# Optimization experiments

Measured on AMD Instinct MI355X. Metric: run time of the kernel, lower is better.

Reference implementation:

```python
import jax, jax.numpy as jnp
import numpy as np

N_NODES = 50000
N_EDGES = 800000
D = 64
LN_EPS = 1e-5


def setup_inputs() -> dict:
    key = jax.random.key(0)
    k1, k2, k3 = jax.random.split(key, 3)
    x = jax.random.normal(k1, (N_NODES, D), dtype=jnp.float32)
    edge_index = jax.random.randint(k2, (2, N_EDGES), 0, N_NODES, dtype=jnp.int64)
    # GCNConv linear weight (no bias in lin; conv bias separate), kaiming-ish scale
    W = jax.random.normal(k3, (D, D), dtype=jnp.float32) / np.sqrt(D)
    b = jnp.zeros((D,), dtype=jnp.float32)
    # LayerNorm affine params
    gamma = jnp.ones((D,), dtype=jnp.float32)
    beta = jnp.zeros((D,), dtype=jnp.float32)
    return {"x": x, "edge_index": edge_index, "W": W, "b": b, "gamma": gamma, "beta": beta}


def reference(x, edge_index, W, b, gamma, beta):
    n = x.shape[0]
    # --- GCNConv (normalize=True, improved=False, add_self_loops=True) ---
    loops = jnp.arange(n, dtype=edge_index.dtype)
    src = jnp.concatenate([edge_index[0], loops])  # message sources j
    dst = jnp.concatenate([edge_index[1], loops])  # message targets i
    ew = jnp.ones(src.shape[0], dtype=x.dtype)
    deg = jax.ops.segment_sum(ew, dst, num_segments=n)          # in-degree incl. self-loop
    dinv = jnp.where(deg > 0, jax.lax.rsqrt(jnp.where(deg > 0, deg, 1.0)), 0.0)
    norm = dinv[src] * dinv[dst]                                 # [E+N]
    xw = x @ W                                                   # [N, D]
    z = jax.ops.segment_sum(norm[:, None] * xw[src], dst, num_segments=n) + b
    # --- identity skip connection ---
    h = x + z
    # --- norm_act_drop: LayerNorm + ReLU (dropout_prob=0) ---
    mu = jnp.mean(h, axis=-1, keepdims=True)
    var = jnp.mean((h - mu) ** 2, axis=-1, keepdims=True)
    hn = (h - mu) * jax.lax.rsqrt(var + LN_EPS)
    return jax.nn.relu(hn * gamma + beta)
```

## Files before the change

### kernel.cpp

```cpp
#include <hip/hip_runtime.h>
#include <hip/hip_fp16.h>

#define N_NODES 50000
#define N_EDGES 800000
#define D 64
#define LN_EPS 1e-5f
#define CAP 48
#define SENT 50000
#define PREP_NB ((N_EDGES / 4 + 255) / 256)
#define GEMM_NB ((N_NODES + 63) / 64)
#define CNT_PAD 50048
#define XS_ROWS 50008
#define NRG 8
#define RSPAN2 6250
#define NCH2 64
#define CHSZ2 12500
#define SC_EB 782

typedef unsigned short u16;
typedef unsigned int u32;


__global__ __launch_bounds__(256) void prep_gemm_k(const int* __restrict__ src,
                                                   const int* __restrict__ dst,
                                                   u32* __restrict__ pe,
                                                   const float* __restrict__ x,
                                                   const float* __restrict__ W,
                                                   __half* __restrict__ xs) {
    __shared__ float xlds[D * D];
    int bid = blockIdx.x;
    int tid = threadIdx.x;
    if (bid < PREP_NB) {
        int gid = bid * 256 + tid;
        if (gid < N_EDGES / 4) {
            int4 s = ((const int4*)src)[gid];
            int4 d = ((const int4*)dst)[gid];
            uint4 p;
            p.x = (u32)(u16)d.x | ((u32)(u16)s.x << 16);
            p.y = (u32)(u16)d.y | ((u32)(u16)s.y << 16);
            p.z = (u32)(u16)d.z | ((u32)(u16)s.z << 16);
            p.w = (u32)(u16)d.w | ((u32)(u16)s.w << 16);
            ((uint4*)pe)[gid] = p;
        }
    } else {
        int row0 = (bid - PREP_NB) * 64;
        const float4* xg = (const float4*)(x + (size_t)row0 * D);
        float4* xl4 = (float4*)xlds;
        for (int i = tid; i < D * D / 4; i += 256) {
            int grow = row0 + (i >> 4);
            xl4[i] = (grow < N_NODES) ? xg[i] : make_float4(0.f, 0.f, 0.f, 0.f);
        }
        int lane = tid & 63;
        float wcol[D];
#pragma unroll
        for (int k = 0; k < D; ++k) wcol[k] = W[k * D + lane];
        __syncthreads();
        int wv = tid >> 6;
        for (int rr = 0; rr < 16; ++rr) {
            int r = wv * 16 + rr;
            int grow = row0 + r;
            if (grow >= N_NODES + 1) break;
            const float4* xr = (const float4*)(xlds + r * D);
            float acc = 0.f;
#pragma unroll
            for (int k4 = 0; k4 < 16; ++k4) {
                float4 xv = xr[k4];
                acc += xv.x * wcol[k4 * 4 + 0];
                acc += xv.y * wcol[k4 * 4 + 1];
                acc += xv.z * wcol[k4 * 4 + 2];
                acc += xv.w * wcol[k4 * 4 + 3];
            }
            xs[(size_t)grow * D + lane] = __float2half(acc);
        }
    }
}

__global__ __launch_bounds__(256) void hist_k(const u32* __restrict__ pe,
                                              u16* __restrict__ lpos,
                                              u16* __restrict__ H) {
    __shared__ u32 lh[RSPAN2];
    int r = blockIdx.x & (NRG - 1);
    int c = blockIdx.x >> 3;
    int lo = r * RSPAN2;
    for (int w = threadIdx.x; w < RSPAN2; w += 256) lh[w] = 0;
    __syncthreads();
    int cbase = c * CHSZ2;
    for (int i = 0; i < 49; ++i) {
        int e = cbase + i * 256 + threadIdx.x;
        if (e < cbase + CHSZ2) {
            u32 p = pe[e];
            unsigned tr = (p & 0xffffu) - (unsigned)lo;
            if (tr < RSPAN2) {
                u32 old = atomicAdd(&lh[tr], 1u);
                lpos[e] = (u16)old;
            }
        }
    }
    __syncthreads();
    u32* H32 = (u32*)(H + (size_t)c * N_NODES + lo);
    for (int w = threadIdx.x; w < RSPAN2 / 2; w += 256)
        H32[w] = (lh[2 * w] & 0xffffu) | (lh[2 * w + 1] << 16);
}

__global__ __launch_bounds__(256) void pref_k(u16* __restrict__ H,
                                              int* __restrict__ cnt) {
    int n = blockIdx.x * 256 + threadIdx.x;
    bool ok = (n < N_NODES);
    u32 v[NCH2];
#pragma unroll
    for (int c = 0; c < NCH2; ++c)
        v[c] = ok ? (u32)H[(size_t)c * N_NODES + n] : 0;
    u32 run = 0;
#pragma unroll
    for (int c = 0; c < NCH2; ++c) { u32 t = v[c]; v[c] = run; run += t; }
    if (ok) {
#pragma unroll
        for (int c = 0; c < NCH2; ++c)
            H[(size_t)c * N_NODES + n] = (u16)v[c];
        cnt[n] = (int)run;
    }
}

__global__ __launch_bounds__(256) void scatter_scale_k(const u32* __restrict__ pe,
                                                       const u16* __restrict__ lpos,
                                                       const u16* __restrict__ H,
                                                       const int* __restrict__ cnt,
                                                       u16* __restrict__ ssrc,
                                                       __half* __restrict__ xs) {
    int bid = blockIdx.x;
    if (bid < SC_EB) {
        int e4 = bid * 1024 + threadIdx.x * 4;
        if (e4 >= N_EDGES) return;
        uint4 p = ((const uint4*)pe)[e4 >> 2];
        ushort4 lp = ((const ushort4*)lpos)[e4 >> 2];
        int c = e4 / CHSZ2;
        const u16* st = H + (size_t)c * N_NODES;
        u32 pp[4] = {p.x, p.y, p.z, p.w};
        u16 ll[4] = {lp.x, lp.y, lp.z, lp.w};
#pragma unroll
        for (int k = 0; k < 4; ++k) {
            int t = (int)(pp[k] & 0xffffu);
            int pos = (int)st[t] + (int)ll[k];
            if (pos < CAP) ssrc[(size_t)t * CAP + pos] = (u16)(pp[k] >> 16);
        }
    } else {
        int gid = (bid - SC_EB) * 256 + threadIdx.x;
        if (gid >= N_NODES * 8) return;
        int row = gid >> 3;
        float di = rsqrtf((float)cnt[row] + 1.0f);
        float4 raw = ((const float4*)xs)[gid];
        __half2* hp = (__half2*)&raw;
#pragma unroll
        for (int i = 0; i < 4; ++i) {
            float2 f = __half22float2(hp[i]);
            hp[i] = __floats2half2_rn(di * f.x, di * f.y);
        }
        ((float4*)xs)[gid] = raw;
    }
}

__global__ __launch_bounds__(256) void agg_ln_k(
        const float* __restrict__ x, const __half* __restrict__ xs,
        const int* __restrict__ cnt, const u16* __restrict__ ssrc,
        const float* __restrict__ b, const float* __restrict__ gamma,
        const float* __restrict__ beta, float* __restrict__ out) {
    int row = blockIdx.x * 4 + (threadIdx.x >> 6);
    if (row >= N_NODES) return;
    int lane = threadIdx.x & 63;
    int sub = lane >> 3;
    int c8  = lane & 7;
    size_t base = (size_t)row * CAP;

    int dc = cnt[row];
    int s0 = ssrc[base + sub + 0];
    int s1 = ssrc[base + sub + 8];
    int s2 = ssrc[base + sub + 16];
    int s3 = ssrc[base + sub + 24];
    int s4 = ssrc[base + sub + 32];
    int s5 = ssrc[base + sub + 40];
    const float4* xp = (const float4*)(x + (size_t)row * D + c8 * 8);
    float4 x0 = xp[0], x1 = xp[1];
    float4 xsr = make_float4(0.f, 0.f, 0.f, 0.f);
    if (sub == 0) xsr = *(const float4*)(xs + (size_t)row * D + c8 * 8);

    int deg = dc < CAP ? dc : CAP;
    int ns = (deg + 7) >> 3;

    int v0 = (sub +  0 < deg) ? s0 : SENT;
    int v1 = (sub +  8 < deg) ? s1 : SENT;
    int v2 = (sub + 16 < deg) ? s2 : SENT;
    int v3 = (sub + 24 < deg) ? s3 : SENT;
    int v4 = (sub + 32 < deg) ? s4 : SENT;
    int v5 = (sub + 40 < deg) ? s5 : SENT;

    float4 r0 = make_float4(0.f,0.f,0.f,0.f), r1 = r0, r2 = r0,
           r3 = r0, r4 = r0, r5 = r0;
    if (0 < ns) r0 = *(const float4*)(xs + (size_t)v0 * D + c8 * 8);
    if (1 < ns) r1 = *(const float4*)(xs + (size_t)v1 * D + c8 * 8);
    if (2 < ns) r2 = *(const float4*)(xs + (size_t)v2 * D + c8 * 8);
    if (3 < ns) r3 = *(const float4*)(xs + (size_t)v3 * D + c8 * 8);
    if (4 < ns) r4 = *(const float4*)(xs + (size_t)v4 * D + c8 * 8);
    if (5 < ns) r5 = *(const float4*)(xs + (size_t)v5 * D + c8 * 8);

    float di = rsqrtf((float)dc + 1.0f);

    float4 a0 = make_float4(0.f, 0.f, 0.f, 0.f);
    float4 a1 = make_float4(0.f, 0.f, 0.f, 0.f);
    {
        float4 rr[7] = {r0, r1, r2, r3, r4, r5, xsr};
#pragma unroll
        for (int k = 0; k < 7; ++k) {
            const __half2* hp = (const __half2*)&rr[k];
            float2 p0 = __half22float2(hp[0]), p1 = __half22float2(hp[1]);
            float2 p2 = __half22float2(hp[2]), p3 = __half22float2(hp[3]);
            a0.x += p0.x; a0.y += p0.y; a0.z += p1.x; a0.w += p1.y;
            a1.x += p2.x; a1.y += p2.y; a1.z += p3.x; a1.w += p3.y;
        }
    }

#pragma unroll
    for (int o = 8; o < 64; o <<= 1) {
        a0.x += __shfl_xor(a0.x, o, 64); a0.y += __shfl_xor(a0.y, o, 64);
        a0.z += __shfl_xor(a0.z, o, 64); a0.w += __shfl_xor(a0.w, o, 64);
        a1.x += __shfl_xor(a1.x, o, 64); a1.y += __shfl_xor(a1.y, o, 64);
        a1.z += __shfl_xor(a1.z, o, 64); a1.w += __shfl_xor(a1.w, o, 64);
    }

    const float4* bp = (const float4*)(b + c8 * 8);
    float4 b0 = bp[0], b1 = bp[1];

    float h[8];
    h[0] = x0.x + di * a0.x + b0.x;
    h[1] = x0.y + di * a0.y + b0.y;
    h[2] = x0.z + di * a0.z + b0.z;
    h[3] = x0.w + di * a0.w + b0.w;
    h[4] = x1.x + di * a1.x + b1.x;
    h[5] = x1.y + di * a1.y + b1.y;
    h[6] = x1.z + di * a1.z + b1.z;
    h[7] = x1.w + di * a1.w + b1.w;

    float s_ = 0.f;
#pragma unroll
    for (int i = 0; i < 8; ++i) s_ += h[i];
#pragma unroll
    for (int o = 1; o < 64; o <<= 1) s_ += __shfl_xor(s_, o, 64);
    float mu = s_ * (1.0f / 512.0f);
    float v_ = 0.f;
    float dd[8];
#pragma unroll
    for (int i = 0; i < 8; ++i) { dd[i] = h[i] - mu; v_ += dd[i] * dd[i]; }
#pragma unroll
    for (int o = 1; o < 64; o <<= 1) v_ += __shfl_xor(v_, o, 64);
    float rstd = rsqrtf(v_ * (1.0f / 512.0f) + LN_EPS);

    if (sub == 0) {
        const float4* gp = (const float4*)(gamma + c8 * 8);
        const float4* ep = (const float4*)(beta + c8 * 8);
        float4 g0 = gp[0], g1 = gp[1];
        float4 e0 = ep[0], e1 = ep[1];
        float4 w0, w1;
        w0.x = fmaxf(dd[0] * rstd * g0.x + e0.x, 0.f);
        w0.y = fmaxf(dd[1] * rstd * g0.y + e0.y, 0.f);
        w0.z = fmaxf(dd[2] * rstd * g0.z + e0.z, 0.f);
        w0.w = fmaxf(dd[3] * rstd * g0.w + e0.w, 0.f);
        w1.x = fmaxf(dd[4] * rstd * g1.x + e1.x, 0.f);
        w1.y = fmaxf(dd[5] * rstd * g1.y + e1.y, 0.f);
        w1.z = fmaxf(dd[6] * rstd * g1.z + e1.z, 0.f);
        w1.w = fmaxf(dd[7] * rstd * g1.w + e1.w, 0.f);
        float4* op = (float4*)(out + (size_t)row * D + c8 * 8);
        op[0] = w0;
        op[1] = w1;
    }
}

extern "C" void kernel_launch(void* const* d_in, const int* in_sizes, int n_in,
                              void* d_out, int out_size, void* d_ws, size_t ws_size,
                              hipStream_t stream) {
    const float* x     = (const float*)d_in[0];
    const int*   ei    = (const int*)d_in[1];
    const float* W     = (const float*)d_in[2];
    const float* b     = (const float*)d_in[3];
    const float* gamma = (const float*)d_in[4];
    const float* beta  = (const float*)d_in[5];
    float* out = (float*)d_out;

    const int* src = ei;
    const int* dst = ei + N_EDGES;

    int*    cnt  = (int*)d_ws;
    __half* xs   = (__half*)(cnt + CNT_PAD);
    u32*    pe   = (u32*)(xs + (size_t)XS_ROWS * D);
    u16*    ssrc = (u16*)(pe + N_EDGES);
    u16*    H    = ssrc + (size_t)N_NODES * CAP;
    u16*    lpos = H + (size_t)NCH2 * N_NODES;

    prep_gemm_k<<<PREP_NB + GEMM_NB, 256, 0, stream>>>(src, dst, pe, x, W, xs);
    hist_k<<<NRG * NCH2, 256, 0, stream>>>(pe, lpos, H);
    pref_k<<<(N_NODES + 255) / 256, 256, 0, stream>>>(H, cnt);
    scatter_scale_k<<<SC_EB + (N_NODES * 8 + 255) / 256, 256, 0, stream>>>(
        pe, lpos, H, cnt, ssrc, xs);
    agg_ln_k<<<(N_NODES + 3) / 4, 256, 0, stream>>>(x, xs, cnt, ssrc, b, gamma, beta, out);
}
```

Baseline: 164.8 us.

## Merge histogram into prep/GEMM kernel and fuse degree scaling into prefix pass

The histogram pass now reads dst directly and runs in the same launch as edge packing and the X·W GEMM, so it no longer waits for the packed edge array. Degree scaling of xs moves into the prefix-sum kernel, using the per-node counts held in shared memory, and the scatter becomes its own kernel. This takes one launch and one dependency stage out of the chain. In exchange, the histogram reads 4-byte dst values instead of packed words, the prefix kernel does more work per block, and the workspace layout is reordered.

```diff
diff --git a/kernel.cpp b/kernel.cpp
--- a/kernel.cpp
+++ b/kernel.cpp
@@ -7,31 +7,86 @@
 #define LN_EPS 1e-5f
 #define CAP 48
 #define SENT 50000
-#define PREP_NB ((N_EDGES / 4 + 255) / 256)
-#define GEMM_NB ((N_NODES + 63) / 64)
 #define CNT_PAD 50048
 #define XS_ROWS 50008
 #define NRG 8
 #define RSPAN2 6250
 #define NCH2 64
 #define CHSZ2 12500
+#define HIST_NB (NRG * NCH2)
+#define GEMM_NB ((N_NODES + 63) / 64)
+#define PREP_NB ((N_EDGES / 4 + 255) / 256)
 #define SC_EB 782
 
 typedef unsigned short u16;
 typedef unsigned int u32;
 
 
-__global__ __launch_bounds__(256) void prep_gemm_k(const int* __restrict__ src,
-                                                   const int* __restrict__ dst,
-                                                   u32* __restrict__ pe,
-                                                   const float* __restrict__ x,
-                                                   const float* __restrict__ W,
-                                                   __half* __restrict__ xs) {
-    __shared__ float xlds[D * D];
+__global__ __launch_bounds__(256) void indep_k(const int* __restrict__ src,
+                                               const int* __restrict__ dst,
+                                               u32* __restrict__ pe,
+                                               u16* __restrict__ lpos,
+                                               u16* __restrict__ H,
+                                               const float* __restrict__ x,
+                                               const float* __restrict__ W,
+                                               __half* __restrict__ xs) {
+    __shared__ u32 smem[RSPAN2];
     int bid = blockIdx.x;
     int tid = threadIdx.x;
-    if (bid < PREP_NB) {
-        int gid = bid * 256 + tid;
+    if (bid < HIST_NB) {
+        int r = bid & (NRG - 1);
+        int c = bid >> 3;
+        int lo = r * RSPAN2;
+        for (int w = tid; w < RSPAN2; w += 256) smem[w] = 0;
+        __syncthreads();
+        int cbase = c * CHSZ2;
+        for (int i = 0; i < 49; ++i) {
+            int e = cbase + i * 256 + tid;
+            if (e < cbase + CHSZ2) {
+                unsigned tr = (unsigned)dst[e] - (unsigned)lo;
+                if (tr < RSPAN2) {
+                    u32 old = atomicAdd(&smem[tr], 1u);
+                    lpos[e] = (u16)old;
+                }
+            }
+        }
+        __syncthreads();
+        u32* H32 = (u32*)(H + (size_t)c * N_NODES + lo);
+        for (int w = tid; w < RSPAN2 / 2; w += 256)
+            H32[w] = (smem[2 * w] & 0xffffu) | (smem[2 * w + 1] << 16);
+    } else if (bid < HIST_NB + GEMM_NB) {
+        float* xlds = (float*)smem;
+        int row0 = (bid - HIST_NB) * 64;
+        const float4* xg = (const float4*)(x + (size_t)row0 * D);
+        float4* xl4 = (float4*)xlds;
+        for (int i = tid; i < D * D / 4; i += 256) {
+            int grow = row0 + (i >> 4);
+            xl4[i] = (grow < N_NODES) ? xg[i] : make_float4(0.f, 0.f, 0.f, 0.f);
+        }
+        int lane = tid & 63;
+        float wcol[D];
+#pragma unroll
+        for (int k = 0; k < D; ++k) wcol[k] = W[k * D + lane];
+        __syncthreads();
+        int wv = tid >> 6;
+        for (int rr = 0; rr < 16; ++rr) {
+            int rloc = wv * 16 + rr;
+            int grow = row0 + rloc;
+            if (grow >= N_NODES + 1) break;
+            const float4* xr = (const float4*)(xlds + rloc * D);
+            float acc = 0.f;
+#pragma unroll
+            for (int k4 = 0; k4 < 16; ++k4) {
+                float4 xv = xr[k4];
+                acc += xv.x * wcol[k4 * 4 + 0];
+                acc += xv.y * wcol[k4 * 4 + 1];
+                acc += xv.z * wcol[k4 * 4 + 2];
+                acc += xv.w * wcol[k4 * 4 + 3];
+            }
+            xs[(size_t)grow * D + lane] = __float2half(acc);
+        }
+    } else {
+        int gid = (bid - HIST_NB - GEMM_NB) * 256 + tid;
         if (gid < N_EDGES / 4) {
             int4 s = ((const int4*)src)[gid];
             int4 d = ((const int4*)dst)[gid];
@@ -42,69 +97,15 @@
             p.w = (u32)(u16)d.w | ((u32)(u16)s.w << 16);
             ((uint4*)pe)[gid] = p;
         }
-    } else {
-        int row0 = (bid - PREP_NB) * 64;
-        const float4* xg = (const float4*)(x + (size_t)row0 * D);
-        float4* xl4 = (float4*)xlds;
-        for (int i = tid; i < D * D / 4; i += 256) {
-            int grow = row0 + (i >> 4);
-            xl4[i] = (grow < N_NODES) ? xg[i] : make_float4(0.f, 0.f, 0.f, 0.f);
-        }
-        int lane = tid & 63;
-        float wcol[D];
-#pragma unroll
-        for (int k = 0; k < D; ++k) wcol[k] = W[k * D + lane];
-        __syncthreads();
-        int wv = tid >> 6;
-        for (int rr = 0; rr < 16; ++rr) {
-            int r = wv * 16 + rr;
-            int grow = row0 + r;
-            if (grow >= N_NODES + 1) break;
-            const float4* xr = (const float4*)(xlds + r * D);
-            float acc = 0.f;
-#pragma unroll
-            for (int k4 = 0; k4 < 16; ++k4) {
-                float4 xv = xr[k4];
-                acc += xv.x * wcol[k4 * 4 + 0];
-                acc += xv.y * wcol[k4 * 4 + 1];
-                acc += xv.z * wcol[k4 * 4 + 2];
-                acc += xv.w * wcol[k4 * 4 + 3];
-            }
-            xs[(size_t)grow * D + lane] = __float2half(acc);
-        }
-    }
-}
-
-__global__ __launch_bounds__(256) void hist_k(const u32* __restrict__ pe,
-                                              u16* __restrict__ lpos,
-                                              u16* __restrict__ H) {
-    __shared__ u32 lh[RSPAN2];
-    int r = blockIdx.x & (NRG - 1);
-    int c = blockIdx.x >> 3;
-    int lo = r * RSPAN2;
-    for (int w = threadIdx.x; w < RSPAN2; w += 256) lh[w] = 0;
-    __syncthreads();
-    int cbase = c * CHSZ2;
-    for (int i = 0; i < 49; ++i) {
-        int e = cbase + i * 256 + threadIdx.x;
-        if (e < cbase + CHSZ2) {
-            u32 p = pe[e];
-            unsigned tr = (p & 0xffffu) - (unsigned)lo;
-            if (tr < RSPAN2) {
-                u32 old = atomicAdd(&lh[tr], 1u);
-                lpos[e] = (u16)old;
-            }
-        }
-    }
-    __syncthreads();
-    u32* H32 = (u32*)(H + (size_t)c * N_NODES + lo);
-    for (int w = threadIdx.x; w < RSPAN2 / 2; w += 256)
-        H32[w] = (lh[2 * w] & 0xffffu) | (lh[2 * w + 1] << 16);
-}
-
-__global__ __launch_bounds__(256) void pref_k(u16* __restrict__ H,
-                                              int* __restrict__ cnt) {
-    int n = blockIdx.x * 256 + threadIdx.x;
+    }
+}
+
+__global__ __launch_bounds__(256) void pref_scale_k(u16* __restrict__ H,
+                                                    int* __restrict__ cnt,
+                                                    __half* __restrict__ xs) {
+    __shared__ float sdi[256];
+    int n0 = blockIdx.x * 256;
+    int n = n0 + threadIdx.x;
     bool ok = (n < N_NODES);
     u32 v[NCH2];
 #pragma unroll
@@ -119,43 +120,46 @@
             H[(size_t)c * N_NODES + n] = (u16)v[c];
         cnt[n] = (int)run;
     }
-}
-
-__global__ __launch_bounds__(256) void scatter_scale_k(const u32* __restrict__ pe,
-                                                       const u16* __restrict__ lpos,
-                                                       const u16* __restrict__ H,
-                                                       const int* __restrict__ cnt,
-                                                       u16* __restrict__ ssrc,
-                                                       __half* __restrict__ xs) {
-    int bid = blockIdx.x;
-    if (bid < SC_EB) {
-        int e4 = bid * 1024 + threadIdx.x * 4;
-        if (e4 >= N_EDGES) return;
-        uint4 p = ((const uint4*)pe)[e4 >> 2];
-        ushort4 lp = ((const ushort4*)lpos)[e4 >> 2];
-        int c = e4 / CHSZ2;
-        const u16* st = H + (size_t)c * N_NODES;
-        u32 pp[4] = {p.x, p.y, p.z, p.w};
-        u16 ll[4] = {lp.x, lp.y, lp.z, lp.w};
-#pragma unroll
-        for (int k = 0; k < 4; ++k) {
-            int t = (int)(pp[k] & 0xffffu);
-            int pos = (int)st[t] + (int)ll[k];
-            if (pos < CAP) ssrc[(size_t)t * CAP + pos] = (u16)(pp[k] >> 16);
-        }
-    } else {
-        int gid = (bid - SC_EB) * 256 + threadIdx.x;
-        if (gid >= N_NODES * 8) return;
-        int row = gid >> 3;
-        float di = rsqrtf((float)cnt[row] + 1.0f);
-        float4 raw = ((const float4*)xs)[gid];
-        __half2* hp = (__half2*)&raw;
-#pragma unroll
-        for (int i = 0; i < 4; ++i) {
-            float2 f = __half22float2(hp[i]);
-            hp[i] = __floats2half2_rn(di * f.x, di * f.y);
-        }
-        ((float4*)xs)[gid] = raw;
+    sdi[threadIdx.x] = rsqrtf((float)run + 1.0f);
+    __syncthreads();
+    float4* xs4 = (float4*)xs;
+#pragma unroll
+    for (int j = 0; j < 8; ++j) {
+        int idx = threadIdx.x + j * 256;
+        int lrow = idx >> 3;
+        int row = n0 + lrow;
+        if (row < N_NODES) {
+            float di = sdi[lrow];
+            size_t g4 = (size_t)row * 8 + (idx & 7);
+            float4 raw = xs4[g4];
+            __half2* hp = (__half2*)&raw;
+#pragma unroll
+            for (int i = 0; i < 4; ++i) {
+                float2 f = __half22float2(hp[i]);
+                hp[i] = __floats2half2_rn(di * f.x, di * f.y);
+            }
+            xs4[g4] = raw;
+        }
+    }
+}
+
+__global__ __launch_bounds__(256) void scatter_k(const u32* __restrict__ pe,
+                                                 const u16* __restrict__ lpos,
+                                                 const u16* __restrict__ H,
+                                                 u16* __restrict__ ssrc) {
+    int e4 = blockIdx.x * 1024 + threadIdx.x * 4;
+    if (e4 >= N_EDGES) return;
+    uint4 p = ((const uint4*)pe)[e4 >> 2];
+    ushort4 lp = ((const ushort4*)lpos)[e4 >> 2];
+    int c = e4 / CHSZ2;
+    const u16* st = H + (size_t)c * N_NODES;
+    u32 pp[4] = {p.x, p.y, p.z, p.w};
+    u16 ll[4] = {lp.x, lp.y, lp.z, lp.w};
+#pragma unroll
+    for (int k = 0; k < 4; ++k) {
+        int t = (int)(pp[k] & 0xffffu);
+        int pos = (int)st[t] + (int)ll[k];
+        if (pos < CAP) ssrc[(size_t)t * CAP + pos] = (u16)(pp[k] >> 16);
     }
 }
 
@@ -290,14 +294,13 @@
     int*    cnt  = (int*)d_ws;
     __half* xs   = (__half*)(cnt + CNT_PAD);
     u32*    pe   = (u32*)(xs + (size_t)XS_ROWS * D);
-    u16*    ssrc = (u16*)(pe + N_EDGES);
-    u16*    H    = ssrc + (size_t)N_NODES * CAP;
+    u16*    H    = (u16*)(pe + N_EDGES);
     u16*    lpos = H + (size_t)NCH2 * N_NODES;
-
-    prep_gemm_k<<<PREP_NB + GEMM_NB, 256, 0, stream>>>(src, dst, pe, x, W, xs);
-    hist_k<<<NRG * NCH2, 256, 0, stream>>>(pe, lpos, H);
-    pref_k<<<(N_NODES + 255) / 256, 256, 0, stream>>>(H, cnt);
-    scatter_scale_k<<<SC_EB + (N_NODES * 8 + 255) / 256, 256, 0, stream>>>(
-        pe, lpos, H, cnt, ssrc, xs);
+    u16*    ssrc = lpos + N_EDGES;
+
+    indep_k<<<HIST_NB + GEMM_NB + PREP_NB, 256, 0, stream>>>(
+        src, dst, pe, lpos, H, x, W, xs);
+    pref_scale_k<<<(N_NODES + 255) / 256, 256, 0, stream>>>(H, cnt, xs);
+    scatter_k<<<SC_EB, 256, 0, stream>>>(pe, lpos, H, ssrc);
     agg_ln_k<<<(N_NODES + 3) / 4, 256, 0, stream>>>(x, xs, cnt, ssrc, b, gamma, beta, out);
 }
```

Measured after the change: 163.0 us. About the same (-1.1%).
